# Kernel tuning notes

Measured on AMD Instinct MI355X. Metric: run time of the kernel, lower is better.

The kernel has to match this reference:

```python
import jax, jax.numpy as jnp
import numpy as np

B, S, N_LM, MAX_LEN = 32, 384, 543, 384

_FACE = [33, 133, 362, 263, 61, 291, 199, 419, 17, 84, 314, 405, 320, 307, 375, 321, 308, 324, 318]
_SEL = np.array(_FACE + list(range(468, 489)) + list(range(522, 543)) + [11, 12, 13, 14, 15, 16], dtype=np.int32)  # 67 landmarks
# pairwise distance index pairs: i in range(3), j in i+1..min(i+3, L)
_PAIRS = [(0, 1), (0, 2), (1, 2), (1, 3), (2, 3), (2, 4)]


def setup_inputs() -> dict:
    key = jax.random.key(0)
    x = jax.random.normal(key, (B, S, N_LM, 3), dtype=jnp.float32)
    return {"x": x}


def _safe_norm(v):
    # torch.norm(v + 1e-8, dim=-1, keepdim=True)
    w = v + 1e-8
    return jnp.sqrt(jnp.sum(w * w, axis=-1, keepdims=True))


def reference(x):
    # select 67 landmarks, keep xy only (z never enters the feature stack)
    c = x[:, :, _SEL, :2]                                  # (B,S,67,2)
    # per-frame masked mean-centering (inputs are finite -> plain mean)
    c = c - jnp.mean(c, axis=2, keepdims=True)
    # per-frame std over flattened (L*2) values, unbiased (torch.std)
    bsz, seq, L, _ = c.shape
    std = jnp.std(c.reshape(bsz, seq, -1), axis=-1, ddof=1)  # (B,S)
    scale = jnp.where(std > 1e-6, 1.0 / std, 1.0)[:, :, None, None]
    c = c * scale                                          # (B,S,67,2)

    zrow = jnp.zeros((bsz, 1, L, 2), c.dtype)
    vel = jnp.concatenate([zrow, c[:, 1:] - c[:, :-1]], axis=1)
    acc = jnp.concatenate([jnp.zeros((bsz, 2, L, 2), c.dtype), vel[:, 2:] - vel[:, 1:-1]], axis=1)

    vm = _safe_norm(vel)                                   # (B,S,67,1)
    am = _safe_norm(acc)
    # cum[t] = sum_{k<t} vm[k]
    cum = jnp.concatenate([jnp.zeros((bsz, 1, L, 1), c.dtype), jnp.cumsum(vm[:, :-1], axis=1)], axis=1)

    ang = jnp.arctan2(vel[..., 1:2] + 1e-8, vel[..., 0:1] + 1e-8)
    dchg = jnp.concatenate([jnp.zeros((bsz, 2, L, 1), c.dtype), ang[:, 2:] - ang[:, 1:-1]], axis=1)

    dists = jnp.concatenate([_safe_norm(c[:, :, i] - c[:, :, j]) for i, j in _PAIRS], axis=-1)  # (B,S,6)

    flat = lambda a: a.reshape(bsz, seq, -1)
    feats = jnp.concatenate([flat(c), flat(vel), flat(acc), flat(vm), flat(am), flat(cum), flat(ang), flat(dchg), dists], axis=-1)
    feats = jnp.where(jnp.isfinite(feats), feats, 0.0)
    return feats[:, :MAX_LEN]
```

## Files before the change

kernel.cpp:

```cpp
#include <hip/hip_runtime.h>
#include <math.h>

#define NB 32
#define NS 384
#define NLM 543
#define NL 67
#define NF 743

__constant__ int d_SEL[NL] = {
    33, 133, 362, 263, 61, 291, 199, 419, 17, 84, 314, 405, 320, 307, 375, 321, 308, 324, 318,
    468, 469, 470, 471, 472, 473, 474, 475, 476, 477, 478, 479, 480, 481, 482, 483, 484, 485, 486, 487, 488,
    522, 523, 524, 525, 526, 527, 528, 529, 530, 531, 532, 533, 534, 535, 536, 537, 538, 539, 540, 541, 542,
    11, 12, 13, 14, 15, 16
};

__device__ __forceinline__ float fin(float v) { return isfinite(v) ? v : 0.0f; }


__global__ __launch_bounds__(256) void k_norm(const float* __restrict__ x,
                                              float* __restrict__ out) {
    const int wave = threadIdx.x >> 6;
    const int lane = threadIdx.x & 63;
    const int bs = blockIdx.x * 4 + wave;
    const float* __restrict__ xr = x + (size_t)bs * (NLM * 3);

    const int lm0 = lane;
    const bool has1 = (lane < 3);
    const int lm1 = lane + 64;

    int o0 = d_SEL[lm0] * 3;
    float a0x = xr[o0], a0y = xr[o0 + 1];
    float a1x = 0.f, a1y = 0.f;
    if (has1) { int o1 = d_SEL[lm1] * 3; a1x = xr[o1]; a1y = xr[o1 + 1]; }

    float sx = a0x + a1x, sy = a0y + a1y;
    #pragma unroll
    for (int off = 32; off; off >>= 1) { sx += __shfl_xor(sx, off); sy += __shfl_xor(sy, off); }
    const float mx = sx * (1.0f / 67.0f), my = sy * (1.0f / 67.0f);

    float c0x = a0x - mx, c0y = a0y - my;
    float c1x = a1x - mx, c1y = a1y - my;

    float ss = c0x * c0x + c0y * c0y + (has1 ? (c1x * c1x + c1y * c1y) : 0.f);
    #pragma unroll
    for (int off = 32; off; off >>= 1) ss += __shfl_xor(ss, off);
    const float stdv = sqrtf(ss * (1.0f / 133.0f));
    const float scale = (stdv > 1e-6f) ? (1.0f / stdv) : 1.0f;

    c0x *= scale; c0y *= scale; c1x *= scale; c1y *= scale;

    float* __restrict__ row = out + (size_t)bs * NF;
    row[2 * lm0]     = fin(c0x);
    row[2 * lm0 + 1] = fin(c0y);
    if (has1) { row[2 * lm1] = fin(c1x); row[2 * lm1 + 1] = fin(c1y); }

    const int PI_[6] = {0, 0, 1, 1, 2, 2};
    const int PJ_[6] = {1, 2, 2, 3, 3, 4};
    const int p = (lane < 6) ? lane : 0;
    float xi = __shfl(c0x, PI_[p]); float yi = __shfl(c0y, PI_[p]);
    float xj = __shfl(c0x, PJ_[p]); float yj = __shfl(c0y, PJ_[p]);
    if (lane < 6) {
        float dx = xi - xj + 1e-8f, dy = yi - yj + 1e-8f;
        row[737 + lane] = fin(sqrtf(dx * dx + dy * dy));
    }
}

__global__ __launch_bounds__(256) void k_dyn(float* __restrict__ out) {
    const unsigned tid = blockIdx.x * 256u + threadIdx.x;
    const unsigned bs = tid / NL;
    const int lm = (int)(tid - bs * NL);
    const int s = (int)(bs % NS);

    float* __restrict__ row = out + (size_t)bs * NF;
    const float cx = row[2 * lm], cy = row[2 * lm + 1];
    float px = 0.f, py = 0.f, qx = 0.f, qy = 0.f;
    if (s >= 1) { px = row[2 * lm - NF];     py = row[2 * lm + 1 - NF]; }
    if (s >= 2) { qx = row[2 * lm - 2 * NF]; qy = row[2 * lm + 1 - 2 * NF]; }

    const float vx = (s >= 1) ? (cx - px) : 0.f;
    const float vy = (s >= 1) ? (cy - py) : 0.f;
    const float v1x = px - qx, v1y = py - qy;
    const float ax = (s >= 2) ? (vx - v1x) : 0.f;
    const float ay = (s >= 2) ? (vy - v1y) : 0.f;

    const float wx = vx + 1e-8f, wy = vy + 1e-8f;
    const float vm = sqrtf(wx * wx + wy * wy);
    const float ux = ax + 1e-8f, uy = ay + 1e-8f;
    const float am = sqrtf(ux * ux + uy * uy);

    const float ang = atan2f(vy + 1e-8f, vx + 1e-8f);
    float dchg = 0.f;
    if (s >= 2) {
        const float ang1 = atan2f(v1y + 1e-8f, v1x + 1e-8f);
        dchg = ang - ang1;
    }

    row[134 + 2 * lm] = vx;
    row[135 + 2 * lm] = vy;
    row[268 + 2 * lm] = ax;
    row[269 + 2 * lm] = ay;
    row[402 + lm] = vm;
    row[469 + lm] = am;
    row[603 + lm] = fin(ang);
    row[670 + lm] = fin(dchg);
}

__global__ __launch_bounds__(256) void k_cum(float* __restrict__ out) {
    const int gw = (int)((blockIdx.x * 256u + threadIdx.x) >> 6);
    const int lane = threadIdx.x & 63;
    const int b = gw / NL;
    const int lm = gw - b * NL;

    float carry = 0.f;
    #pragma unroll
    for (int k = 0; k < 6; ++k) {
        const int t = k * 64 + lane;
        const size_t idx = ((size_t)(b * NS + t)) * NF;
        const float v = out[idx + 402 + lm];
        float incl = v;
        #pragma unroll
        for (int off = 1; off < 64; off <<= 1) {
            float y = __shfl_up(incl, off);
            if (lane >= off) incl += y;
        }
        out[idx + 536 + lm] = fin(carry + (incl - v));
        carry += __shfl(incl, 63);
    }
}

extern "C" void kernel_launch(void* const* d_in, const int* in_sizes, int n_in,
                              void* d_out, int out_size, void* d_ws, size_t ws_size,
                              hipStream_t stream) {
    const float* x = (const float*)d_in[0];
    float* out = (float*)d_out;

    k_norm<<<(NB * NS) / 4, 256, 0, stream>>>(x, out);
    k_dyn<<<(NB * NS * NL) / 256, 256, 0, stream>>>(out);
    k_cum<<<(NB * NL) / 4, 256, 0, stream>>>(out);
}
```

Baseline: 137.0 us.

## Fuse normalization and dynamics kernels by recomputing previous frames per wave

Merges the normalization and velocity/acceleration kernels into one. Each wave re-gathers and re-normalizes the two previous frames from the input instead of reading normalized values back from the output. Velocity magnitudes are also written to a contiguous per-landmark workspace, so the cumulative-sum scan reads coalesced data instead of strided output rows. This removes one launch and the output round-trip, at the cost of three times the gather and reduction work per frame.

```diff
diff --git a/kernel.cpp b/kernel.cpp
--- a/kernel.cpp
+++ b/kernel.cpp
@@ -17,29 +17,21 @@
 __device__ __forceinline__ float fin(float v) { return isfinite(v) ? v : 0.0f; }
 
 
-__global__ __launch_bounds__(256) void k_norm(const float* __restrict__ x,
-                                              float* __restrict__ out) {
-    const int wave = threadIdx.x >> 6;
-    const int lane = threadIdx.x & 63;
-    const int bs = blockIdx.x * 4 + wave;
-    const float* __restrict__ xr = x + (size_t)bs * (NLM * 3);
-
-    const int lm0 = lane;
-    const bool has1 = (lane < 3);
-    const int lm1 = lane + 64;
-
-    int o0 = d_SEL[lm0] * 3;
+__device__ __forceinline__ void gather_norm(const float* __restrict__ xr,
+                                            int lane, int o0, int o1, bool has1,
+                                            float& c0x, float& c0y,
+                                            float& c1x, float& c1y) {
     float a0x = xr[o0], a0y = xr[o0 + 1];
     float a1x = 0.f, a1y = 0.f;
-    if (has1) { int o1 = d_SEL[lm1] * 3; a1x = xr[o1]; a1y = xr[o1 + 1]; }
+    if (has1) { a1x = xr[o1]; a1y = xr[o1 + 1]; }
 
     float sx = a0x + a1x, sy = a0y + a1y;
     #pragma unroll
     for (int off = 32; off; off >>= 1) { sx += __shfl_xor(sx, off); sy += __shfl_xor(sy, off); }
     const float mx = sx * (1.0f / 67.0f), my = sy * (1.0f / 67.0f);
 
-    float c0x = a0x - mx, c0y = a0y - my;
-    float c1x = a1x - mx, c1y = a1y - my;
+    c0x = a0x - mx; c0y = a0y - my;
+    c1x = a1x - mx; c1y = a1y - my;
 
     float ss = c0x * c0x + c0y * c0y + (has1 ? (c1x * c1x + c1y * c1y) : 0.f);
     #pragma unroll
@@ -48,11 +40,70 @@
     const float scale = (stdv > 1e-6f) ? (1.0f / stdv) : 1.0f;
 
     c0x *= scale; c0y *= scale; c1x *= scale; c1y *= scale;
+}
+
+__global__ __launch_bounds__(256) void k_main(const float* __restrict__ x,
+                                              float* __restrict__ out,
+                                              float* __restrict__ vmstage) {
+    const int wave = threadIdx.x >> 6;
+    const int lane = threadIdx.x & 63;
+    const int bs = blockIdx.x * 4 + wave;
+    const int s = bs % NS;
+    const int b = bs / NS;
+
+    const int lm0 = lane;
+    const bool has1 = (lane < 3);
+    const int lm1 = lane + 64;
+    const int o0 = d_SEL[lm0] * 3;
+    const int o1 = has1 ? d_SEL[lm1] * 3 : 0;
+
+    const float* __restrict__ xr = x + (size_t)bs * (NLM * 3);
+
+    float c0x, c0y, c1x, c1y;
+    gather_norm(xr, lane, o0, o1, has1, c0x, c0y, c1x, c1y);
+
+    float p0x = 0.f, p0y = 0.f, p1x = 0.f, p1y = 0.f;
+    if (s >= 1) gather_norm(xr - NLM * 3, lane, o0, o1, has1, p0x, p0y, p1x, p1y);
+    float q0x = 0.f, q0y = 0.f, q1x = 0.f, q1y = 0.f;
+    if (s >= 2) gather_norm(xr - 2 * NLM * 3, lane, o0, o1, has1, q0x, q0y, q1x, q1y);
 
     float* __restrict__ row = out + (size_t)bs * NF;
-    row[2 * lm0]     = fin(c0x);
-    row[2 * lm0 + 1] = fin(c0y);
-    if (has1) { row[2 * lm1] = fin(c1x); row[2 * lm1 + 1] = fin(c1y); }
+
+    #pragma unroll
+    for (int half = 0; half < 2; ++half) {
+        if (half == 1 && !has1) break;
+        const int lm  = half ? lm1 : lm0;
+        const float cx = half ? c1x : c0x, cy = half ? c1y : c0y;
+        const float px = half ? p1x : p0x, py = half ? p1y : p0y;
+        const float qx = half ? q1x : q0x, qy = half ? q1y : q0y;
+
+        const float vx = (s >= 1) ? (cx - px) : 0.f;
+        const float vy = (s >= 1) ? (cy - py) : 0.f;
+        const float v1x = px - qx, v1y = py - qy;
+        const float ax = (s >= 2) ? (vx - v1x) : 0.f;
+        const float ay = (s >= 2) ? (vy - v1y) : 0.f;
+
+        const float wx = vx + 1e-8f, wy = vy + 1e-8f;
+        const float vm = sqrtf(wx * wx + wy * wy);
+        const float ux = ax + 1e-8f, uy = ay + 1e-8f;
+        const float am = sqrtf(ux * ux + uy * uy);
+
+        const float ang = atan2f(vy + 1e-8f, vx + 1e-8f);
+        float dchg = 0.f;
+        if (s >= 2) dchg = ang - atan2f(v1y + 1e-8f, v1x + 1e-8f);
+
+        row[2 * lm]       = fin(cx);
+        row[2 * lm + 1]   = fin(cy);
+        row[134 + 2 * lm] = vx;
+        row[135 + 2 * lm] = vy;
+        row[268 + 2 * lm] = ax;
+        row[269 + 2 * lm] = ay;
+        row[402 + lm]     = vm;
+        row[469 + lm]     = am;
+        row[603 + lm]     = fin(ang);
+        row[670 + lm]     = fin(dchg);
+        vmstage[((size_t)b * NL + lm) * NS + s] = vm;
+    }
 
     const int PI_[6] = {0, 0, 1, 1, 2, 2};
     const int PJ_[6] = {1, 2, 2, 3, 3, 4};
@@ -65,65 +116,26 @@
     }
 }
 
-__global__ __launch_bounds__(256) void k_dyn(float* __restrict__ out) {
-    const unsigned tid = blockIdx.x * 256u + threadIdx.x;
-    const unsigned bs = tid / NL;
-    const int lm = (int)(tid - bs * NL);
-    const int s = (int)(bs % NS);
-
-    float* __restrict__ row = out + (size_t)bs * NF;
-    const float cx = row[2 * lm], cy = row[2 * lm + 1];
-    float px = 0.f, py = 0.f, qx = 0.f, qy = 0.f;
-    if (s >= 1) { px = row[2 * lm - NF];     py = row[2 * lm + 1 - NF]; }
-    if (s >= 2) { qx = row[2 * lm - 2 * NF]; qy = row[2 * lm + 1 - 2 * NF]; }
-
-    const float vx = (s >= 1) ? (cx - px) : 0.f;
-    const float vy = (s >= 1) ? (cy - py) : 0.f;
-    const float v1x = px - qx, v1y = py - qy;
-    const float ax = (s >= 2) ? (vx - v1x) : 0.f;
-    const float ay = (s >= 2) ? (vy - v1y) : 0.f;
-
-    const float wx = vx + 1e-8f, wy = vy + 1e-8f;
-    const float vm = sqrtf(wx * wx + wy * wy);
-    const float ux = ax + 1e-8f, uy = ay + 1e-8f;
-    const float am = sqrtf(ux * ux + uy * uy);
-
-    const float ang = atan2f(vy + 1e-8f, vx + 1e-8f);
-    float dchg = 0.f;
-    if (s >= 2) {
-        const float ang1 = atan2f(v1y + 1e-8f, v1x + 1e-8f);
-        dchg = ang - ang1;
-    }
-
-    row[134 + 2 * lm] = vx;
-    row[135 + 2 * lm] = vy;
-    row[268 + 2 * lm] = ax;
-    row[269 + 2 * lm] = ay;
-    row[402 + lm] = vm;
-    row[469 + lm] = am;
-    row[603 + lm] = fin(ang);
-    row[670 + lm] = fin(dchg);
-}
-
-__global__ __launch_bounds__(256) void k_cum(float* __restrict__ out) {
+__global__ __launch_bounds__(256) void k_scan(const float* __restrict__ vmstage,
+                                              float* __restrict__ out) {
     const int gw = (int)((blockIdx.x * 256u + threadIdx.x) >> 6);
     const int lane = threadIdx.x & 63;
     const int b = gw / NL;
     const int lm = gw - b * NL;
+    const float* __restrict__ src = vmstage + (size_t)gw * NS;
 
     float carry = 0.f;
     #pragma unroll
     for (int k = 0; k < 6; ++k) {
         const int t = k * 64 + lane;
-        const size_t idx = ((size_t)(b * NS + t)) * NF;
-        const float v = out[idx + 402 + lm];
+        const float v = src[t];
         float incl = v;
         #pragma unroll
         for (int off = 1; off < 64; off <<= 1) {
             float y = __shfl_up(incl, off);
             if (lane >= off) incl += y;
         }
-        out[idx + 536 + lm] = fin(carry + (incl - v));
+        out[((size_t)(b * NS + t)) * NF + 536 + lm] = fin(carry + (incl - v));
         carry += __shfl(incl, 63);
     }
 }
@@ -133,8 +145,8 @@
                               hipStream_t stream) {
     const float* x = (const float*)d_in[0];
     float* out = (float*)d_out;
+    float* vmstage = (float*)d_ws;
 
-    k_norm<<<(NB * NS) / 4, 256, 0, stream>>>(x, out);
-    k_dyn<<<(NB * NS * NL) / 256, 256, 0, stream>>>(out);
-    k_cum<<<(NB * NL) / 4, 256, 0, stream>>>(out);
+    k_main<<<(NB * NS) / 4, 256, 0, stream>>>(x, out, vmstage);
+    k_scan<<<(NB * NL) / 4, 256, 0, stream>>>(vmstage, out);
 }
```

Result: no change. 136.5 us (-0.4%).
